# Optimization experiments

Measured on AMD Instinct MI355X. Metric: run time of the kernel, lower is better.

Reference implementation:

```python
import jax, jax.numpy as jnp
import numpy as np

N_NODES = 50000
N_EDGES = 800000
D_MODEL = 64
D_EDGE = 32
D_HIDDEN = 256
N_GRAPHS = 64
EPS = 1e-5


def setup_inputs() -> dict:
    key = jax.random.key(0)
    ks = jax.random.split(key, 16)
    h = jax.random.normal(ks[0], (N_NODES, D_MODEL), dtype=jnp.float32)
    edge_index = jax.random.randint(ks[1], (2, N_EDGES), 0, N_NODES, dtype=jnp.int64)
    edge_attr = jax.random.normal(ks[2], (N_EDGES, D_EDGE), dtype=jnp.float32)
    batch = jnp.sort(jax.random.randint(ks[3], (N_NODES,), 0, N_GRAPHS, dtype=jnp.int64))
    s_in = 1.0 / np.sqrt(2 * D_MODEL + D_EDGE)
    s_h = 1.0 / np.sqrt(D_HIDDEN)
    s_u = 1.0 / np.sqrt(2 * D_MODEL)
    return {
        "h": h,
        "edge_attr": edge_attr,
        "edge_index": edge_index,
        "batch": batch,
        "msg_w1": jax.random.normal(ks[4], (2 * D_MODEL + D_EDGE, D_HIDDEN), dtype=jnp.float32) * s_in,
        "msg_b1": jnp.zeros((D_HIDDEN,), dtype=jnp.float32),
        "msg_w2": jax.random.normal(ks[5], (D_HIDDEN, D_MODEL), dtype=jnp.float32) * s_h,
        "msg_b2": jnp.zeros((D_MODEL,), dtype=jnp.float32),
        "upd_w1": jax.random.normal(ks[6], (2 * D_MODEL, D_HIDDEN), dtype=jnp.float32) * s_u,
        "upd_b1": jnp.zeros((D_HIDDEN,), dtype=jnp.float32),
        "upd_w2": jax.random.normal(ks[7], (D_HIDDEN, D_MODEL), dtype=jnp.float32) * s_h,
        "upd_b2": jnp.zeros((D_MODEL,), dtype=jnp.float32),
        "gn_weight": jnp.ones((D_MODEL,), dtype=jnp.float32),
        "gn_bias": jnp.zeros((D_MODEL,), dtype=jnp.float32),
        "gn_alpha": jnp.ones((D_MODEL,), dtype=jnp.float32),
    }


def _graph_norm(h, batch, weight, bias, alpha):
    # GraphNorm: subtract alpha-scaled per-graph mean, divide by per-graph std.
    ones = jnp.ones((h.shape[0],), dtype=h.dtype)
    counts = jax.ops.segment_sum(ones, batch, num_segments=N_GRAPHS)
    counts = jnp.maximum(counts, 1.0)[:, None]  # [G, 1]
    mean = jax.ops.segment_sum(h, batch, num_segments=N_GRAPHS) / counts  # [G, d]
    h_c = h - alpha * mean[batch]  # [N, d]
    var = jax.ops.segment_sum(h_c * h_c, batch, num_segments=N_GRAPHS) / counts  # [G, d]
    return weight * h_c / jnp.sqrt(var[batch] + EPS) + bias


def reference(h, edge_attr, edge_index, batch,
              msg_w1, msg_b1, msg_w2, msg_b2,
              upd_w1, upd_b1, upd_w2, upd_b2,
              gn_weight, gn_bias, gn_alpha):
    src, dst = edge_index[0], edge_index[1]
    # m_ij = MLP([h_dst, h_src, e_ij])   (dropout inactive in eval mode)
    m_in = jnp.concatenate([h[dst], h[src], edge_attr], axis=-1)  # [E, 2d+de]
    m = jax.nn.silu(m_in @ msg_w1 + msg_b1) @ msg_w2 + msg_b2      # [E, d]
    # agg_i = sum over incoming edges
    agg = jax.ops.segment_sum(m, dst, num_segments=h.shape[0])     # [N, d]
    # h_i' = h_i + MLP([h_i, agg_i])
    upd_in = jnp.concatenate([h, agg], axis=-1)                    # [N, 2d]
    dh = jax.nn.silu(upd_in @ upd_w1 + upd_b1) @ upd_w2 + upd_b2   # [N, d]
    h = h + dh
    return _graph_norm(h, batch, gn_weight, gn_bias, gn_alpha)
```

## Files before the change

kernel.cpp:

```cpp
#include <hip/hip_runtime.h>
#include <hip/hip_bf16.h>
#include <stdint.h>

#define N_NODES   50000
#define N_EDGES   800000
#define D_MODEL   64
#define D_HIDDEN  256
#define N_GRAPHS  64
#define EPS_GN    1e-5f

#define NBINS_PAD 50176
#define NB_SCAN   196

typedef __attribute__((ext_vector_type(8))) short short8;
typedef __attribute__((ext_vector_type(4))) float f32x4;
typedef __attribute__((ext_vector_type(4))) float float4v;
typedef __attribute__((ext_vector_type(2))) unsigned int uint2v;
typedef __attribute__((ext_vector_type(4))) unsigned int uint4v;

static __device__ __forceinline__ short f2bf(float f) {
  union { float f; uint32_t u; } v; v.f = f;
  uint32_t r = (v.u + 0x7fffu + ((v.u >> 16) & 1u)) >> 16;
  return (short)(uint16_t)r;
}

static __device__ __forceinline__ uint32_t pack_bf16x2(float lo, float hi) {
  union { float f; uint32_t u; } a, b;
  a.f = lo; b.f = hi;
  uint32_t ra = a.u + 0x7fffu + ((a.u >> 16) & 1u);
  uint32_t rb = b.u + 0x7fffu + ((b.u >> 16) & 1u);
  return __builtin_amdgcn_perm(rb, ra, 0x07060302u);
}

static __device__ __forceinline__ uint32_t cvt_pk_bf16(float lo, float hi) {
  uint32_t r;
  asm("v_cvt_pk_bf16_f32 %0, %1, %2" : "=v"(r) : "v"(lo), "v"(hi));
  return r;
}

static __device__ __forceinline__ float silu_f(float x) {
  return x * __builtin_amdgcn_rcpf(1.0f + __expf(-x));
}

static __device__ __forceinline__ f32x4 mfma16(short8 a, short8 b, f32x4 c) {
  return __builtin_amdgcn_mfma_f32_16x16x32_bf16(a, b, c, 0, 0, 0);
}

#define HBF_BLOCKS 1563

__global__ void prep_all(const float* __restrict__ mw1, const float* __restrict__ mw2,
                         const float* __restrict__ uw1, const float* __restrict__ uw2,
                         const float* __restrict__ h,
                         short* __restrict__ w1f, short* __restrict__ w2f,
                         short* __restrict__ u1f, short* __restrict__ u2f,
                         short* __restrict__ h_bf) {
  int b = blockIdx.x;
  if (b >= 52) {
    int t2 = (b - 52) * 256 + threadIdx.x;
    if (t2 < N_NODES * D_MODEL / 8) {
      const float4v* src = (const float4v*)(h + (size_t)t2 * 8);
      float4v v0 = src[0], v1 = src[1];
      uint4v p = {pack_bf16x2(v0.x, v0.y), pack_bf16x2(v0.z, v0.w),
                  pack_bf16x2(v1.x, v1.y), pack_bf16x2(v1.z, v1.w)};
      *(uint4v*)(h_bf + (size_t)t2 * 8) = p;
    }
    return;
  }
  const float* w; short* out; int K, Nn, t;
  if (b < 20)      { w = mw1; out = w1f; K = 160; Nn = 256; t = b * 256 + threadIdx.x; }
  else if (b < 28) { w = mw2; out = w2f; K = 256; Nn = 64;  t = (b - 20) * 256 + threadIdx.x; }
  else if (b < 44) { w = uw1; out = u1f; K = 128; Nn = 256; t = (b - 28) * 256 + threadIdx.x; }
  else             { w = uw2; out = u2f; K = 256; Nn = 64;  t = (b - 44) * 256 + threadIdx.x; }
  int total = (K >> 5) * (Nn >> 4) * 64;
  if (t >= total) return;
  const bool permK = (K == 256);
  int lane = t & 63;
  int rest = t >> 6;
  int ntN = Nn >> 4;
  int nt = rest % ntN;
  int kt = rest / ntN;
  int n  = nt * 16 + (lane & 15);
  int k0 = kt * 32 + (lane >> 4) * 8;
  short* o = out + (size_t)t * 8;
#pragma unroll
  for (int j = 0; j < 8; ++j) {
    int kk = k0 + j;
    int kr = permK ? ((kk >> 6) * 4 + (kk & 3)) * 16 + ((kk >> 2) & 15) : kk;
    o[j] = f2bf(w[(size_t)kr * Nn + n]);
  }
}

__global__ __launch_bounds__(256)
void hist_k(const int* __restrict__ ei, int* __restrict__ hist) {
  int e = blockIdx.x * 256 + threadIdx.x;
  if (e >= N_EDGES) return;
  atomicAdd(&hist[ei[N_EDGES + e]], 1);
}

__global__ __launch_bounds__(256)
void scan1(const int* __restrict__ hist, int* __restrict__ offs,
           int* __restrict__ bsums) {
  __shared__ int tmp[256];
  int i = blockIdx.x * 256 + threadIdx.x;
  int v = hist[i];
  tmp[threadIdx.x] = v;
  __syncthreads();
#pragma unroll
  for (int d = 1; d < 256; d <<= 1) {
    int t = (threadIdx.x >= d) ? tmp[threadIdx.x - d] : 0;
    __syncthreads();
    tmp[threadIdx.x] += t;
    __syncthreads();
  }
  offs[i] = tmp[threadIdx.x] - v;
  if (threadIdx.x == 255) bsums[blockIdx.x] = tmp[255];
}

__global__ __launch_bounds__(256)
void scan2(const int* __restrict__ bsums, int* __restrict__ bpre) {
  __shared__ int tmp[256];
  int v = (threadIdx.x < NB_SCAN) ? bsums[threadIdx.x] : 0;
  tmp[threadIdx.x] = v;
  __syncthreads();
#pragma unroll
  for (int d = 1; d < 256; d <<= 1) {
    int t = (threadIdx.x >= d) ? tmp[threadIdx.x - d] : 0;
    __syncthreads();
    tmp[threadIdx.x] += t;
    __syncthreads();
  }
  bpre[threadIdx.x] = tmp[threadIdx.x] - v;
}

__global__ __launch_bounds__(256)
void scan3(int* __restrict__ offs, const int* __restrict__ bpre) {
  int i = blockIdx.x * 256 + threadIdx.x;
  offs[i] += bpre[blockIdx.x];
}

__global__ __launch_bounds__(256)
void scatter_k(const int* __restrict__ ei, int* __restrict__ offs,
               int* __restrict__ sorted) {
  int e = blockIdx.x * 256 + threadIdx.x;
  if (e >= N_EDGES) return;
  int d = ei[N_EDGES + e];
  int pos = atomicAdd(&offs[d], 1);
  sorted[pos] = e;
}

#define LDA_E 168
#define LDH   264
#define LDC   68

__global__ __launch_bounds__(256, 2)
void edge_mlp(const short* __restrict__ h_bf, const float* __restrict__ ea,
              const int* __restrict__ ei, const int* __restrict__ sorted,
              const short* __restrict__ w1f, const float* __restrict__ b1,
              const short* __restrict__ w2f, const float* __restrict__ b2,
              float* __restrict__ agg) {
  __shared__ __align__(16) short buf[64 * LDH];
  __shared__ __align__(16) float sC[64 * LDC];
  __shared__ int s_ids[4][48];

  const int tid  = threadIdx.x;
  const int lane = tid & 63;
  const int wave = tid >> 6;
  const int col  = lane & 15;
  const int quad = lane >> 4;
  const int eb   = blockIdx.x * 64 + wave * 16;
  short* sA = buf;
  short* sH = buf;

  if (lane < 48) {
    int i15 = lane & 15;
    int e0 = sorted[eb + i15];
    int v;
    if (lane < 16)      v = ei[e0];
    else if (lane < 32) v = ei[N_EDGES + e0];
    else                v = e0;
    s_ids[wave][lane] = v;
  }

#pragma unroll
  for (int it = 0; it < 2; ++it) {
    int idx = it * 64 + lane;
    int e = idx >> 3, c = idx & 7;
    int row = wave * 16 + e;
    int d = s_ids[wave][16 + e];
    int s = s_ids[wave][e];
    *(short8*)&sA[row * LDA_E + c * 8] =
        *(const short8*)(h_bf + (size_t)d * D_MODEL + c * 8);
    *(short8*)&sA[row * LDA_E + 64 + c * 8] =
        *(const short8*)(h_bf + (size_t)s * D_MODEL + c * 8);
  }
#pragma unroll
  for (int it = 0; it < 2; ++it) {
    int idx = it * 64 + lane;
    int e = idx >> 3, j = idx & 7;
    int row = wave * 16 + e;
    int eid = s_ids[wave][32 + e];
    float4v v = *(const float4v*)(ea + (size_t)eid * 32 + j * 4);
    uint2v p = {pack_bf16x2(v.x, v.y), pack_bf16x2(v.z, v.w)};
    *(uint2v*)&sA[row * LDA_E + 128 + j * 4] = p;
  }
  __syncthreads();

  f32x4 acc[4][4];
#pragma unroll
  for (int mt = 0; mt < 4; ++mt)
#pragma unroll
    for (int nt = 0; nt < 4; ++nt)
      acc[mt][nt] = (f32x4){0.f, 0.f, 0.f, 0.f};

  short8 bf[2][4];
#pragma unroll
  for (int nt = 0; nt < 4; ++nt)
    bf[0][nt] = *(const short8*)(w1f + (size_t)((wave * 4 + nt) * 64 + lane) * 8);

#pragma unroll
  for (int kt = 0; kt < 5; ++kt) {
    if (kt < 4) {
#pragma unroll
      for (int nt = 0; nt < 4; ++nt)
        bf[(kt + 1) & 1][nt] = *(const short8*)(
            w1f + (size_t)(((kt + 1) * 16 + wave * 4 + nt) * 64 + lane) * 8);
    }
    short8 af[4];
#pragma unroll
    for (int mt = 0; mt < 4; ++mt)
      af[mt] = *(const short8*)&sA[(mt * 16 + col) * LDA_E + kt * 32 + quad * 8];
#pragma unroll
    for (int nt = 0; nt < 4; ++nt)
#pragma unroll
      for (int mt = 0; mt < 4; ++mt)
        acc[mt][nt] = mfma16(af[mt], bf[kt & 1][nt], acc[mt][nt]);
  }
  __syncthreads();

  {
    float b1v[4];
#pragma unroll
    for (int nt = 0; nt < 4; ++nt) b1v[nt] = b1[(wave * 4 + nt) * 16 + col];
#pragma unroll
    for (int mt = 0; mt < 4; ++mt) {
#pragma unroll
      for (int r = 0; r < 4; ++r) {
        const int row = mt * 16 + quad * 4 + r;
        float v0 = silu_f(acc[mt][0][r] + b1v[0]);
        float v1 = silu_f(acc[mt][1][r] + b1v[1]);
        float v2 = silu_f(acc[mt][2][r] + b1v[2]);
        float v3 = silu_f(acc[mt][3][r] + b1v[3]);
        uint2v p = {cvt_pk_bf16(v0, v1), cvt_pk_bf16(v2, v3)};
        *(uint2v*)&sH[row * LDH + wave * 64 + col * 4] = p;
      }
    }
  }
  __syncthreads();

  f32x4 acc2[4];
#pragma unroll
  for (int mt = 0; mt < 4; ++mt) acc2[mt] = (f32x4){0.f, 0.f, 0.f, 0.f};

  short8 bf2[2];
  bf2[0] = *(const short8*)(w2f + (size_t)(wave * 64 + lane) * 8);

#pragma unroll
  for (int kt = 0; kt < 8; ++kt) {
    if (kt < 7)
      bf2[(kt + 1) & 1] = *(const short8*)(
          w2f + (size_t)(((kt + 1) * 4 + wave) * 64 + lane) * 8);
    short8 af[4];
#pragma unroll
    for (int mt = 0; mt < 4; ++mt)
      af[mt] = *(const short8*)&sH[(mt * 16 + col) * LDH + kt * 32 + quad * 8];
#pragma unroll
    for (int mt = 0; mt < 4; ++mt)
      acc2[mt] = mfma16(af[mt], bf2[kt & 1], acc2[mt]);
  }

  {
    const int n = wave * 16 + col;
    const float bias = b2[n];
#pragma unroll
    for (int mt = 0; mt < 4; ++mt)
#pragma unroll
      for (int r = 0; r < 4; ++r)
        sC[(mt * 16 + quad * 4 + r) * LDC + n] = acc2[mt][r] + bias;
  }
  __syncthreads();

  {
    float sum = 0.f;
    int prev = s_ids[wave][16];
#pragma unroll
    for (int r = 0; r < 16; ++r) {
      float v = sC[(wave * 16 + r) * LDC + lane];
      int d = s_ids[wave][16 + r];
      if (d != prev) {
        atomicAdd(agg + (size_t)prev * D_MODEL + lane, sum);
        sum = 0.f; prev = d;
      }
      sum += v;
    }
    atomicAdd(agg + (size_t)prev * D_MODEL + lane, sum);
  }
}

#define LDA_N 136

__global__ __launch_bounds__(256, 2)
void node_mlp(const float* __restrict__ h, const short* __restrict__ h_bf,
              const float* __restrict__ agg,
              const short* __restrict__ w1f, const float* __restrict__ b1,
              const short* __restrict__ w2f, const float* __restrict__ b2,
              const int* __restrict__ batch,
              float* __restrict__ hnew,
              float* __restrict__ s1, float* __restrict__ s2,
              float* __restrict__ cnt) {
  __shared__ __align__(16) short buf[64 * LDH];
  __shared__ int s_b[64];

  const int tid  = threadIdx.x;
  const int lane = tid & 63;
  const int wave = tid >> 6;
  const int col  = lane & 15;
  const int quad = lane >> 4;
  const int nb   = blockIdx.x * 64;
  short* sA = buf;
  short* sH = buf;

  if (tid < 64) {
    int gi = nb + tid;
    s_b[tid] = batch[(gi < N_NODES) ? gi : (N_NODES - 1)];
  }

#pragma unroll
  for (int it = 0; it < 2; ++it) {
    int idx = it * 64 + lane;
    int i = idx >> 3, c = idx & 7;
    int row = wave * 16 + i;
    int gi = nb + row;
    if (gi >= N_NODES) gi = N_NODES - 1;
    *(short8*)&sA[row * LDA_N + c * 8] =
        *(const short8*)(h_bf + (size_t)gi * D_MODEL + c * 8);
  }
#pragma unroll
  for (int it = 0; it < 4; ++it) {
    int idx = it * 64 + lane;
    int i = idx >> 4, j = idx & 15;
    int row = wave * 16 + i;
    int gi = nb + row;
    if (gi >= N_NODES) gi = N_NODES - 1;
    float4v v = *(const float4v*)(agg + (size_t)gi * D_MODEL + j * 4);
    uint2v p = {pack_bf16x2(v.x, v.y), pack_bf16x2(v.z, v.w)};
    *(uint2v*)&sA[row * LDA_N + 64 + j * 4] = p;
  }
  __syncthreads();

  if (wave == 3) {
    int gi = nb + lane;
    bool valid = gi < N_NODES;
    int g = s_b[lane];
    int gp = __shfl_up(g, 1);
    bool start = valid && (lane == 0 || g != gp);
    unsigned long long bmask = __ballot(start);
    unsigned long long imask = __ballot(!valid);
    if (start) {
      unsigned long long higher =
          (lane == 63) ? 0ULL : (((bmask | imask) >> (lane + 1)) << (lane + 1));
      int next = higher ? (__ffsll((long long)higher) - 1) : 64;
      atomicAdd(&cnt[g], (float)(next - lane));
    }
  }

  f32x4 acc[4][4];
#pragma unroll
  for (int mt = 0; mt < 4; ++mt)
#pragma unroll
    for (int nt = 0; nt < 4; ++nt)
      acc[mt][nt] = (f32x4){0.f, 0.f, 0.f, 0.f};

  short8 bf[2][4];
#pragma unroll
  for (int nt = 0; nt < 4; ++nt)
    bf[0][nt] = *(const short8*)(w1f + (size_t)((wave * 4 + nt) * 64 + lane) * 8);

#pragma unroll
  for (int kt = 0; kt < 4; ++kt) {
    if (kt < 3) {
#pragma unroll
      for (int nt = 0; nt < 4; ++nt)
        bf[(kt + 1) & 1][nt] = *(const short8*)(
            w1f + (size_t)(((kt + 1) * 16 + wave * 4 + nt) * 64 + lane) * 8);
    }
    short8 af[4];
#pragma unroll
    for (int mt = 0; mt < 4; ++mt)
      af[mt] = *(const short8*)&sA[(mt * 16 + col) * LDA_N + kt * 32 + quad * 8];
#pragma unroll
    for (int nt = 0; nt < 4; ++nt)
#pragma unroll
      for (int mt = 0; mt < 4; ++mt)
        acc[mt][nt] = mfma16(af[mt], bf[kt & 1][nt], acc[mt][nt]);
  }
  __syncthreads();

  {
    float b1v[4];
#pragma unroll
    for (int nt = 0; nt < 4; ++nt) b1v[nt] = b1[(wave * 4 + nt) * 16 + col];
#pragma unroll
    for (int mt = 0; mt < 4; ++mt) {
#pragma unroll
      for (int r = 0; r < 4; ++r) {
        const int row = mt * 16 + quad * 4 + r;
        float v0 = silu_f(acc[mt][0][r] + b1v[0]);
        float v1 = silu_f(acc[mt][1][r] + b1v[1]);
        float v2 = silu_f(acc[mt][2][r] + b1v[2]);
        float v3 = silu_f(acc[mt][3][r] + b1v[3]);
        uint2v p = {cvt_pk_bf16(v0, v1), cvt_pk_bf16(v2, v3)};
        *(uint2v*)&sH[row * LDH + wave * 64 + col * 4] = p;
      }
    }
  }
  __syncthreads();

  f32x4 acc2[4];
#pragma unroll
  for (int mt = 0; mt < 4; ++mt) acc2[mt] = (f32x4){0.f, 0.f, 0.f, 0.f};

  short8 bf2[2];
  bf2[0] = *(const short8*)(w2f + (size_t)(wave * 64 + lane) * 8);

#pragma unroll
  for (int kt = 0; kt < 8; ++kt) {
    if (kt < 7)
      bf2[(kt + 1) & 1] = *(const short8*)(
          w2f + (size_t)(((kt + 1) * 4 + wave) * 64 + lane) * 8);
    short8 af[4];
#pragma unroll
    for (int mt = 0; mt < 4; ++mt)
      af[mt] = *(const short8*)&sH[(mt * 16 + col) * LDH + kt * 32 + quad * 8];
#pragma unroll
    for (int mt = 0; mt < 4; ++mt)
      acc2[mt] = mfma16(af[mt], bf2[kt & 1], acc2[mt]);
  }

  {
    const int n = wave * 16 + col;
    const float bias = b2[n];
    float a1 = 0.f, a2 = 0.f;
    int prev = s_b[quad * 4];
#pragma unroll
    for (int mt = 0; mt < 4; ++mt) {
#pragma unroll
      for (int r = 0; r < 4; ++r) {
        const int row = mt * 16 + quad * 4 + r;
        const int gi = nb + row;
        const bool valid = gi < N_NODES;
        int g = s_b[row];
        if (g != prev) {
          atomicAdd(&s1[prev * D_MODEL + n], a1);
          atomicAdd(&s2[prev * D_MODEL + n], a2);
          a1 = 0.f; a2 = 0.f; prev = g;
        }
        if (valid) {
          float hv = h[(size_t)gi * D_MODEL + n] + acc2[mt][r] + bias;
          hnew[(size_t)gi * D_MODEL + n] = hv;
          a1 += hv; a2 += hv * hv;
        }
      }
    }
    atomicAdd(&s1[prev * D_MODEL + n], a1);
    atomicAdd(&s2[prev * D_MODEL + n], a2);
  }
}

__global__ __launch_bounds__(256)
void gn_norm(float* __restrict__ x, const int* __restrict__ batch,
             const float* __restrict__ s1, const float* __restrict__ s2,
             const float* __restrict__ cnt, const float* __restrict__ alpha,
             const float* __restrict__ weight, const float* __restrict__ bias) {
  int idx = blockIdx.x * 256 + threadIdx.x;
  if (idx >= N_NODES * D_MODEL) return;
  int i = idx >> 6, f = idx & 63;
  int g = batch[i];
  float c = fmaxf(cnt[g], 1.f);
  float m   = s1[g * D_MODEL + f] / c;
  float ex2 = s2[g * D_MODEL + f] / c;
  float a = alpha[f];
  float var = ex2 - 2.f * a * m * m + a * a * m * m;
  float hc = x[idx] - a * m;
  x[idx] = weight[f] * hc * rsqrtf(var + EPS_GN) + bias[f];
}

extern "C" void kernel_launch(void* const* d_in, const int* in_sizes, int n_in,
                              void* d_out, int out_size, void* d_ws, size_t ws_size,
                              hipStream_t stream) {
  const float* h     = (const float*)d_in[0];
  const float* ea    = (const float*)d_in[1];
  const int*   ei    = (const int*)d_in[2];
  const int*   batch = (const int*)d_in[3];
  const float* mw1   = (const float*)d_in[4];
  const float* mb1   = (const float*)d_in[5];
  const float* mw2   = (const float*)d_in[6];
  const float* mb2   = (const float*)d_in[7];
  const float* uw1   = (const float*)d_in[8];
  const float* ub1   = (const float*)d_in[9];
  const float* uw2   = (const float*)d_in[10];
  const float* ub2   = (const float*)d_in[11];
  const float* gw    = (const float*)d_in[12];
  const float* gb    = (const float*)d_in[13];
  const float* ga    = (const float*)d_in[14];

  char* ws = (char*)d_ws;
  float* agg    = (float*)(ws + 0);
  short* w1f    = (short*)(ws + 12800000);
  short* w2f    = (short*)(ws + 12881920);
  short* u1f    = (short*)(ws + 12914688);
  short* u2f    = (short*)(ws + 12980224);
  float* s1     = (float*)(ws + 13012992);
  float* s2     = (float*)(ws + 13029376);
  float* cnt    = (float*)(ws + 13045760);
  int*   hist   = (int*)  (ws + 13046016);
  int*   offs   = (int*)  (ws + 13246720);
  int*   bsums  = (int*)  (ws + 13447424);
  int*   bpre   = (int*)  (ws + 13448448);
  int*   sorted = (int*)  (ws + 13449472);
  short* h_bf   = (short*)(ws + 16649472);

  hipMemsetAsync(agg, 0, 12800000, stream);
  hipMemsetAsync(ws + 13012992, 0, 33024, stream);
  hipMemsetAsync(hist, 0, 200704, stream);

  prep_all<<<52 + HBF_BLOCKS, 256, 0, stream>>>(mw1, mw2, uw1, uw2, h,
                                                w1f, w2f, u1f, u2f, h_bf);

  hist_k  <<<(N_EDGES + 255) / 256, 256, 0, stream>>>(ei, hist);
  scan1   <<<NB_SCAN, 256, 0, stream>>>(hist, offs, bsums);
  scan2   <<<1, 256, 0, stream>>>(bsums, bpre);
  scan3   <<<NB_SCAN, 256, 0, stream>>>(offs, bpre);
  scatter_k<<<(N_EDGES + 255) / 256, 256, 0, stream>>>(ei, offs, sorted);

  edge_mlp<<<N_EDGES / 64, 256, 0, stream>>>(h_bf, ea, ei, sorted,
                                             w1f, mb1, w2f, mb2, agg);

  node_mlp<<<(N_NODES + 63) / 64, 256, 0, stream>>>(h, h_bf, agg,
                                                    u1f, ub1, u2f, ub2,
                                                    batch, (float*)d_out,
                                                    s1, s2, cnt);

  gn_norm<<<(N_NODES * D_MODEL + 255) / 256, 256, 0, stream>>>(
      (float*)d_out, batch, s1, s2, cnt, ga, gw, gb);
}
```

Measured before the change: 448.1 us.

## Load MFMA A-fragments directly from global memory and fold scan3 into scatter

Edge and node MLP kernels now gather the first-layer A operand fragments straight from global memory into registers instead of staging them through LDS, removing one LDS round-trip and a barrier. The sC buffer is aliased onto the shared hidden buffer, which cuts LDS use and lets the edge kernel raise its occupancy hint to 3 blocks per CU. The scan3 kernel is removed by adding the block prefix inside scatter_k, saving a launch. The direct gathers use fragment-shaped access patterns that may coalesce less well than the previous staged loads.

```diff
diff --git a/kernel.cpp b/kernel.cpp
--- a/kernel.cpp
+++ b/kernel.cpp
@@ -44,6 +44,13 @@
 
 static __device__ __forceinline__ f32x4 mfma16(short8 a, short8 b, f32x4 c) {
   return __builtin_amdgcn_mfma_f32_16x16x32_bf16(a, b, c, 0, 0, 0);
+}
+
+static __device__ __forceinline__ short8 pack8(float4v u0, float4v u1) {
+  union { uint4v u; short8 s; } cv;
+  cv.u = (uint4v){pack_bf16x2(u0.x, u0.y), pack_bf16x2(u0.z, u0.w),
+                  pack_bf16x2(u1.x, u1.y), pack_bf16x2(u1.z, u1.w)};
+  return cv.s;
 }
 
 #define HBF_BLOCKS 1563
@@ -133,33 +140,25 @@
 }
 
 __global__ __launch_bounds__(256)
-void scan3(int* __restrict__ offs, const int* __restrict__ bpre) {
-  int i = blockIdx.x * 256 + threadIdx.x;
-  offs[i] += bpre[blockIdx.x];
-}
-
-__global__ __launch_bounds__(256)
 void scatter_k(const int* __restrict__ ei, int* __restrict__ offs,
-               int* __restrict__ sorted) {
+               const int* __restrict__ bpre, int* __restrict__ sorted) {
   int e = blockIdx.x * 256 + threadIdx.x;
   if (e >= N_EDGES) return;
   int d = ei[N_EDGES + e];
-  int pos = atomicAdd(&offs[d], 1);
+  int pos = atomicAdd(&offs[d], 1) + bpre[d >> 8];
   sorted[pos] = e;
 }
 
-#define LDA_E 168
 #define LDH   264
 #define LDC   68
 
-__global__ __launch_bounds__(256, 2)
+__global__ __launch_bounds__(256, 3)
 void edge_mlp(const short* __restrict__ h_bf, const float* __restrict__ ea,
               const int* __restrict__ ei, const int* __restrict__ sorted,
               const short* __restrict__ w1f, const float* __restrict__ b1,
               const short* __restrict__ w2f, const float* __restrict__ b2,
               float* __restrict__ agg) {
   __shared__ __align__(16) short buf[64 * LDH];
-  __shared__ __align__(16) float sC[64 * LDC];
   __shared__ int s_ids[4][48];
 
   const int tid  = threadIdx.x;
@@ -168,7 +167,6 @@
   const int col  = lane & 15;
   const int quad = lane >> 4;
   const int eb   = blockIdx.x * 64 + wave * 16;
-  short* sA = buf;
   short* sH = buf;
 
   if (lane < 48) {
@@ -180,30 +178,15 @@
     else                v = e0;
     s_ids[wave][lane] = v;
   }
-
-#pragma unroll
-  for (int it = 0; it < 2; ++it) {
-    int idx = it * 64 + lane;
-    int e = idx >> 3, c = idx & 7;
-    int row = wave * 16 + e;
-    int d = s_ids[wave][16 + e];
-    int s = s_ids[wave][e];
-    *(short8*)&sA[row * LDA_E + c * 8] =
-        *(const short8*)(h_bf + (size_t)d * D_MODEL + c * 8);
-    *(short8*)&sA[row * LDA_E + 64 + c * 8] =
-        *(const short8*)(h_bf + (size_t)s * D_MODEL + c * 8);
-  }
-#pragma unroll
-  for (int it = 0; it < 2; ++it) {
-    int idx = it * 64 + lane;
-    int e = idx >> 3, j = idx & 7;
-    int row = wave * 16 + e;
-    int eid = s_ids[wave][32 + e];
-    float4v v = *(const float4v*)(ea + (size_t)eid * 32 + j * 4);
-    uint2v p = {pack_bf16x2(v.x, v.y), pack_bf16x2(v.z, v.w)};
-    *(uint2v*)&sA[row * LDA_E + 128 + j * 4] = p;
-  }
-  __syncthreads();
+  __syncthreads();
+
+  int idd[4], idsr[4], ide[4];
+#pragma unroll
+  for (int mt = 0; mt < 4; ++mt) {
+    idd[mt]  = s_ids[mt][16 + col];
+    idsr[mt] = s_ids[mt][col];
+    ide[mt]  = s_ids[mt][32 + col];
+  }
 
   f32x4 acc[4][4];
 #pragma unroll
@@ -212,30 +195,39 @@
     for (int nt = 0; nt < 4; ++nt)
       acc[mt][nt] = (f32x4){0.f, 0.f, 0.f, 0.f};
 
-  short8 bf[2][4];
+  short8 bfr[2][4];
 #pragma unroll
   for (int nt = 0; nt < 4; ++nt)
-    bf[0][nt] = *(const short8*)(w1f + (size_t)((wave * 4 + nt) * 64 + lane) * 8);
+    bfr[0][nt] = *(const short8*)(w1f + (size_t)((wave * 4 + nt) * 64 + lane) * 8);
 
 #pragma unroll
   for (int kt = 0; kt < 5; ++kt) {
+    short8 af[4];
+#pragma unroll
+    for (int mt = 0; mt < 4; ++mt) {
+      if (kt < 2) {
+        af[mt] = *(const short8*)(h_bf + (size_t)idd[mt] * 64 + kt * 32 + quad * 8);
+      } else if (kt < 4) {
+        af[mt] = *(const short8*)(h_bf + (size_t)idsr[mt] * 64 + (kt - 2) * 32 + quad * 8);
+      } else {
+        const float* p = ea + (size_t)ide[mt] * 32 + quad * 8;
+        float4v u0 = *(const float4v*)p;
+        float4v u1 = *(const float4v*)(p + 4);
+        af[mt] = pack8(u0, u1);
+      }
+    }
     if (kt < 4) {
 #pragma unroll
       for (int nt = 0; nt < 4; ++nt)
-        bf[(kt + 1) & 1][nt] = *(const short8*)(
+        bfr[(kt + 1) & 1][nt] = *(const short8*)(
             w1f + (size_t)(((kt + 1) * 16 + wave * 4 + nt) * 64 + lane) * 8);
     }
-    short8 af[4];
-#pragma unroll
-    for (int mt = 0; mt < 4; ++mt)
-      af[mt] = *(const short8*)&sA[(mt * 16 + col) * LDA_E + kt * 32 + quad * 8];
 #pragma unroll
     for (int nt = 0; nt < 4; ++nt)
 #pragma unroll
       for (int mt = 0; mt < 4; ++mt)
-        acc[mt][nt] = mfma16(af[mt], bf[kt & 1][nt], acc[mt][nt]);
-  }
-  __syncthreads();
+        acc[mt][nt] = mfma16(af[mt], bfr[kt & 1][nt], acc[mt][nt]);
+  }
 
   {
     float b1v[4];
@@ -277,8 +269,10 @@
     for (int mt = 0; mt < 4; ++mt)
       acc2[mt] = mfma16(af[mt], bf2[kt & 1], acc2[mt]);
   }
+  __syncthreads();
 
   {
+    float* sC = (float*)buf;
     const int n = wave * 16 + col;
     const float bias = b2[n];
 #pragma unroll
@@ -290,6 +284,7 @@
   __syncthreads();
 
   {
+    const float* sC = (const float*)buf;
     float sum = 0.f;
     int prev = s_ids[wave][16];
 #pragma unroll
@@ -305,8 +300,6 @@
     atomicAdd(agg + (size_t)prev * D_MODEL + lane, sum);
   }
 }
-
-#define LDA_N 136
 
 __global__ __launch_bounds__(256, 2)
 void node_mlp(const float* __restrict__ h, const short* __restrict__ h_bf,
@@ -326,7 +319,6 @@
   const int col  = lane & 15;
   const int quad = lane >> 4;
   const int nb   = blockIdx.x * 64;
-  short* sA = buf;
   short* sH = buf;
 
   if (tid < 64) {
@@ -334,26 +326,69 @@
     s_b[tid] = batch[(gi < N_NODES) ? gi : (N_NODES - 1)];
   }
 
-#pragma unroll
-  for (int it = 0; it < 2; ++it) {
-    int idx = it * 64 + lane;
-    int i = idx >> 3, c = idx & 7;
-    int row = wave * 16 + i;
-    int gi = nb + row;
-    if (gi >= N_NODES) gi = N_NODES - 1;
-    *(short8*)&sA[row * LDA_N + c * 8] =
-        *(const short8*)(h_bf + (size_t)gi * D_MODEL + c * 8);
-  }
-#pragma unroll
-  for (int it = 0; it < 4; ++it) {
-    int idx = it * 64 + lane;
-    int i = idx >> 4, j = idx & 15;
-    int row = wave * 16 + i;
-    int gi = nb + row;
-    if (gi >= N_NODES) gi = N_NODES - 1;
-    float4v v = *(const float4v*)(agg + (size_t)gi * D_MODEL + j * 4);
-    uint2v p = {pack_bf16x2(v.x, v.y), pack_bf16x2(v.z, v.w)};
-    *(uint2v*)&sA[row * LDA_N + 64 + j * 4] = p;
+  int gi4[4];
+#pragma unroll
+  for (int mt = 0; mt < 4; ++mt) {
+    int g = nb + mt * 16 + col;
+    gi4[mt] = (g < N_NODES) ? g : (N_NODES - 1);
+  }
+
+  f32x4 acc[4][4];
+#pragma unroll
+  for (int mt = 0; mt < 4; ++mt)
+#pragma unroll
+    for (int nt = 0; nt < 4; ++nt)
+      acc[mt][nt] = (f32x4){0.f, 0.f, 0.f, 0.f};
+
+  short8 bfr[2][4];
+#pragma unroll
+  for (int nt = 0; nt < 4; ++nt)
+    bfr[0][nt] = *(const short8*)(w1f + (size_t)((wave * 4 + nt) * 64 + lane) * 8);
+
+#pragma unroll
+  for (int kt = 0; kt < 4; ++kt) {
+    short8 af[4];
+#pragma unroll
+    for (int mt = 0; mt < 4; ++mt) {
+      if (kt < 2) {
+        af[mt] = *(const short8*)(h_bf + (size_t)gi4[mt] * 64 + kt * 32 + quad * 8);
+      } else {
+        const float* p = agg + (size_t)gi4[mt] * 64 + (kt - 2) * 32 + quad * 8;
+        float4v u0 = *(const float4v*)p;
+        float4v u1 = *(const float4v*)(p + 4);
+        af[mt] = pack8(u0, u1);
+      }
+    }
+    if (kt < 3) {
+#pragma unroll
+      for (int nt = 0; nt < 4; ++nt)
+        bfr[(kt + 1) & 1][nt] = *(const short8*)(
+            w1f + (size_t)(((kt + 1) * 16 + wave * 4 + nt) * 64 + lane) * 8);
+    }
+#pragma unroll
+    for (int nt = 0; nt < 4; ++nt)
+#pragma unroll
+      for (int mt = 0; mt < 4; ++mt)
+        acc[mt][nt] = mfma16(af[mt], bfr[kt & 1][nt], acc[mt][nt]);
+  }
+
+  {
+    float b1v[4];
+#pragma unroll
+    for (int nt = 0; nt < 4; ++nt) b1v[nt] = b1[(wave * 4 + nt) * 16 + col];
+#pragma unroll
+    for (int mt = 0; mt < 4; ++mt) {
+#pragma unroll
+      for (int r = 0; r < 4; ++r) {
+        const int row = mt * 16 + quad * 4 + r;
+        float v0 = silu_f(acc[mt][0][r] + b1v[0]);
+        float v1 = silu_f(acc[mt][1][r] + b1v[1]);
+        float v2 = silu_f(acc[mt][2][r] + b1v[2]);
+        float v3 = silu_f(acc[mt][3][r] + b1v[3]);
+        uint2v p = {cvt_pk_bf16(v0, v1), cvt_pk_bf16(v2, v3)};
+        *(uint2v*)&sH[row * LDH + wave * 64 + col * 4] = p;
+      }
+    }
   }
   __syncthreads();
 
@@ -372,58 +407,6 @@
       atomicAdd(&cnt[g], (float)(next - lane));
     }
   }
-
-  f32x4 acc[4][4];
-#pragma unroll
-  for (int mt = 0; mt < 4; ++mt)
-#pragma unroll
-    for (int nt = 0; nt < 4; ++nt)
-      acc[mt][nt] = (f32x4){0.f, 0.f, 0.f, 0.f};
-
-  short8 bf[2][4];
-#pragma unroll
-  for (int nt = 0; nt < 4; ++nt)
-    bf[0][nt] = *(const short8*)(w1f + (size_t)((wave * 4 + nt) * 64 + lane) * 8);
-
-#pragma unroll
-  for (int kt = 0; kt < 4; ++kt) {
-    if (kt < 3) {
-#pragma unroll
-      for (int nt = 0; nt < 4; ++nt)
-        bf[(kt + 1) & 1][nt] = *(const short8*)(
-            w1f + (size_t)(((kt + 1) * 16 + wave * 4 + nt) * 64 + lane) * 8);
-    }
-    short8 af[4];
-#pragma unroll
-    for (int mt = 0; mt < 4; ++mt)
-      af[mt] = *(const short8*)&sA[(mt * 16 + col) * LDA_N + kt * 32 + quad * 8];
-#pragma unroll
-    for (int nt = 0; nt < 4; ++nt)
-#pragma unroll
-      for (int mt = 0; mt < 4; ++mt)
-        acc[mt][nt] = mfma16(af[mt], bf[kt & 1][nt], acc[mt][nt]);
-  }
-  __syncthreads();
-
-  {
-    float b1v[4];
-#pragma unroll
-    for (int nt = 0; nt < 4; ++nt) b1v[nt] = b1[(wave * 4 + nt) * 16 + col];
-#pragma unroll
-    for (int mt = 0; mt < 4; ++mt) {
-#pragma unroll
-      for (int r = 0; r < 4; ++r) {
-        const int row = mt * 16 + quad * 4 + r;
-        float v0 = silu_f(acc[mt][0][r] + b1v[0]);
-        float v1 = silu_f(acc[mt][1][r] + b1v[1]);
-        float v2 = silu_f(acc[mt][2][r] + b1v[2]);
-        float v3 = silu_f(acc[mt][3][r] + b1v[3]);
-        uint2v p = {cvt_pk_bf16(v0, v1), cvt_pk_bf16(v2, v3)};
-        *(uint2v*)&sH[row * LDH + wave * 64 + col * 4] = p;
-      }
-    }
-  }
-  __syncthreads();
 
   f32x4 acc2[4];
 #pragma unroll
@@ -539,8 +522,7 @@
   hist_k  <<<(N_EDGES + 255) / 256, 256, 0, stream>>>(ei, hist);
   scan1   <<<NB_SCAN, 256, 0, stream>>>(hist, offs, bsums);
   scan2   <<<1, 256, 0, stream>>>(bsums, bpre);
-  scan3   <<<NB_SCAN, 256, 0, stream>>>(offs, bpre);
-  scatter_k<<<(N_EDGES + 255) / 256, 256, 0, stream>>>(ei, offs, sorted);
+  scatter_k<<<(N_EDGES + 255) / 256, 256, 0, stream>>>(ei, offs, bpre, sorted);
 
   edge_mlp<<<N_EDGES / 64, 256, 0, stream>>>(h_bf, ea, ei, sorted,
                                              w1f, mb1, w2f, mb2, agg);
```

Result: slower. 515.1 us (+14.9%).
